# Kernel tuning notes

Measured on AMD Instinct MI355X. Metric: run time of the kernel, lower is better.

Reference implementation:

```python
import jax, jax.numpy as jnp
import numpy as np

N = 50000   # nodes
E = 800000  # edges
G = 64      # graphs in batch
H1, D1 = 2, 64   # gat1: 2 heads x 64
D2 = 32          # gat2: 1 head x 32
IN = 1
EPS = 1e-5


def _gat(h, src, dst, W, al, ar, Wres, bias, Hh, D):
    # DGL GATConv (eval mode): project, per-edge attention, edge softmax over dst, scatter-sum, residual + bias
    feat = (h @ W).reshape(N, Hh, D)                     # [N,H,D]
    el = jnp.sum(feat * al, axis=-1)                     # [N,H]
    er = jnp.sum(feat * ar, axis=-1)                     # [N,H]
    e = jax.nn.leaky_relu(el[src] + er[dst], 0.2)        # [E,H]
    m = jax.ops.segment_max(e, dst, num_segments=N)      # [N,H] (stable softmax)
    a = jnp.exp(e - m[dst])
    s = jax.ops.segment_sum(a, dst, num_segments=N)
    alpha = a / s[dst]                                   # [E,H]
    msg = feat[src] * alpha[:, :, None]                  # [E,H,D]
    rst = jax.ops.segment_sum(msg, dst, num_segments=N)  # [N,H,D]
    res = (h @ Wres).reshape(N, Hh, D)
    return rst + res + bias.reshape(1, Hh, D)


def _bn(x, gamma, beta, mean, var):
    return (x - mean) * jax.lax.rsqrt(var + EPS) * gamma + beta


def setup_inputs() -> dict:
    key = jax.random.key(0)
    ks = jax.random.split(key, 32)
    rn = lambda i, shape: jax.random.normal(ks[i], shape, jnp.float32) * 0.1
    inp = {
        'feat': jax.random.normal(ks[0], (N, IN), jnp.float32),
        'W1': rn(1, (IN, H1 * D1)), 'al1': rn(2, (H1, D1)), 'ar1': rn(3, (H1, D1)),
        'res1': rn(4, (IN, H1 * D1)), 'b1': rn(5, (H1 * D1,)),
        'g1_gamma': jnp.ones((H1 * D1,), jnp.float32), 'g1_beta': jnp.zeros((H1 * D1,), jnp.float32),
        'g1_mean': rn(6, (H1 * D1,)), 'g1_var': jax.random.uniform(ks[7], (H1 * D1,), jnp.float32) + 0.5,
        'W2': rn(8, (H1 * D1, D2)), 'al2': rn(9, (1, D2)), 'ar2': rn(10, (1, D2)),
        'res2': rn(11, (H1 * D1, D2)), 'b2': rn(12, (D2,)),
        'g2_gamma': jnp.ones((D2,), jnp.float32), 'g2_beta': jnp.zeros((D2,), jnp.float32),
        'g2_mean': rn(13, (D2,)), 'g2_var': jax.random.uniform(ks[14], (D2,), jnp.float32) + 0.5,
        'Wd1': rn(15, (D2, H1 * D1)), 'bd1': rn(16, (H1 * D1,)),
        'gd_gamma': jnp.ones((H1 * D1,), jnp.float32), 'gd_beta': jnp.zeros((H1 * D1,), jnp.float32),
        'gd_mean': rn(17, (H1 * D1,)), 'gd_var': jax.random.uniform(ks[18], (H1 * D1,), jnp.float32) + 0.5,
        'Wd2': rn(19, (H1 * D1, IN)), 'bd2': rn(20, (IN,)),
        'src': jax.random.randint(ks[21], (E,), 0, N, jnp.int32),
        'dst': jax.random.randint(ks[22], (E,), 0, N, jnp.int32),
        'graph_ids': jnp.sort(jax.random.randint(ks[23], (N,), 0, G, jnp.int32)),
    }
    return inp


def reference(feat, W1, al1, ar1, res1, b1, g1_gamma, g1_beta, g1_mean, g1_var,
              W2, al2, ar2, res2, b2, g2_gamma, g2_beta, g2_mean, g2_var,
              Wd1, bd1, gd_gamma, gd_beta, gd_mean, gd_var, Wd2, bd2,
              src, dst, graph_ids):
    h = _gat(feat, src, dst, W1, al1, ar1, res1, b1, H1, D1)   # [N,2,64]
    h = h.reshape(N, H1 * D1)
    h = jax.nn.relu(_bn(h, g1_gamma, g1_beta, g1_mean, g1_var))
    h = _gat(h, src, dst, W2, al2, ar2, res2, b2, 1, D2)       # [N,1,32]
    h = h.reshape(N, D2)
    h = jax.nn.relu(_bn(h, g2_gamma, g2_beta, g2_mean, g2_var))
    # dgl.mean_nodes over batched graphs
    counts = jax.ops.segment_sum(jnp.ones((N,), h.dtype), graph_ids, num_segments=G)
    graph_rep = jax.ops.segment_sum(h, graph_ids, num_segments=G) / jnp.maximum(counts, 1.0)[:, None]
    # decoder: Linear -> BN -> ReLU -> Linear (dropout off in eval)
    d = jax.nn.relu(_bn(h @ Wd1 + bd1, gd_gamma, gd_beta, gd_mean, gd_var))
    reconstruction = d @ Wd2 + bd2
    return graph_rep, reconstruction
```

## Files before the change

### kernel.cpp

```cpp
#include <hip/hip_runtime.h>
#include <hip/hip_bf16.h>
#include <hip/hip_fp16.h>

#define NN 50000
#define NE 800000
#define NG 64
#define C1 128
#define D2 32
#define CAP 32
#define NRANGE 4
#define RNG 12500
#define NCH 391
#define BN_EPS 1e-5f

#define CST_A   0
#define CST_B   2
#define CST_P   4
#define CST_Q   132
#define CST_R   260
#define CST_SC2 388
#define CST_RC2 420
#define CST_SD  452
#define CST_RD  580
#define CST_N   1024

#define UO_DEGP  0
#define UO_OVFC  800000
#define ZERO_UNITS 800016
#define UO_FLAG  800016
#define UO_CST   800032
#define UO_ESRC2 801056
#define UO_OVF   1601056
#define UO_FCAN  3201056
#define UO_F2    3251056
#define UO_RS2   4051056
#define UO_EL2   5651056
#define UO_ER2   5701056

typedef _Float16 h2vec __attribute__((ext_vector_type(2)));

__device__ __forceinline__ float lrelu(float x) { return fmaxf(x, 0.2f * x); }
__device__ __forceinline__ float bu2f(unsigned int u) {
    union { unsigned int i; float f; } v; v.i = (u & 0xFFFFu) << 16; return v.f;
}
__device__ __forceinline__ unsigned short f2bu(float f) {
    union { float f; unsigned int i; } v; v.f = f;
    unsigned int r = v.i + 0x7FFFu + ((v.i >> 16) & 1u);
    return (unsigned short)(r >> 16);
}
__device__ __forceinline__ unsigned int packh2(float a, float b) {
    h2vec h; h.x = (_Float16)a; h.y = (_Float16)b;
    union { h2vec h; unsigned int u; } v; v.h = h; return v.u;
}
__device__ __forceinline__ h2vec as_h2(unsigned int u) {
    union { unsigned int u; h2vec h; } v; v.u = u; return v.h;
}
__device__ __forceinline__ float ldw(const void* p, int i, int bf) {
    return bf ? bu2f(((const unsigned short*)p)[i]) : ((const float*)p)[i];
}
__device__ __forceinline__ int sniff64(const unsigned int* fw, int l) {
    int cnt = 0;
    for (int j = l; j < 256; j += 64) {
        unsigned int b = (fw[j] >> 8) & 0x7Fu;
        cnt += (b >= 0x3Au && b <= 0x41u) ? 1 : 0;
    }
#pragma unroll
    for (int m = 32; m >= 1; m >>= 1) cnt += __shfl_xor(cnt, m);
    return (cnt > 128) ? 1 : 0;
}

__global__ __launch_bounds__(256) void k_prep(
                       const void* __restrict__ feat, const int* __restrict__ dst,
                       const int* __restrict__ src,
                       float* __restrict__ fcan, int* __restrict__ degp,
                       unsigned short* __restrict__ esrc2,
                       int2* __restrict__ ovf, int* __restrict__ ovfc,
                       const void* W1, const void* al1, const void* ar1,
                       const void* res1, const void* b1,
                       const void* g1g, const void* g1b, const void* g1m, const void* g1v,
                       const void* b2v, const void* g2g, const void* g2b,
                       const void* g2m, const void* g2v,
                       const void* bd1, const void* gdg, const void* gdb,
                       const void* gdm, const void* gdv,
                       int* __restrict__ flag, float* __restrict__ cst) {
    __shared__ int sBf;
    int t = threadIdx.x;
    if (t < 64) {
        int b = sniff64((const unsigned int*)feat, t);
        if (t == 0) sBf = b;
    }
    __syncthreads();
    int bf = sBf;
    int r = blockIdx.x / NCH;
    int c = blockIdx.x % NCH;

    if (blockIdx.x == 0) {
        if (t == 0) *flag = bf;
        if (t < 128) {
            float w1v = ldw(W1, t, bf);
            float pa = w1v * ldw(al1, t, bf);
            float pb = w1v * ldw(ar1, t, bf);
#pragma unroll
            for (int m = 32; m >= 1; m >>= 1) { pa += __shfl_xor(pa, m); pb += __shfl_xor(pb, m); }
            if ((t & 63) == 0) { cst[CST_A + (t >> 6)] = pa; cst[CST_B + (t >> 6)] = pb; }
            float sc = rsqrtf(ldw(g1v, t, bf) + BN_EPS) * ldw(g1g, t, bf);
            cst[CST_P + t] = w1v * sc;
            cst[CST_Q + t] = ldw(res1, t, bf) * sc;
            cst[CST_R + t] = (ldw(b1, t, bf) - ldw(g1m, t, bf)) * sc + ldw(g1b, t, bf);
            if (t < D2) {
                float s2 = rsqrtf(ldw(g2v, t, bf) + BN_EPS) * ldw(g2g, t, bf);
                cst[CST_SC2 + t] = s2;
                cst[CST_RC2 + t] = (ldw(b2v, t, bf) - ldw(g2m, t, bf)) * s2 + ldw(g2b, t, bf);
            }
            float sd = rsqrtf(ldw(gdv, t, bf) + BN_EPS) * ldw(gdg, t, bf);
            cst[CST_SD + t] = sd;
            cst[CST_RD + t] = (ldw(bd1, t, bf) - ldw(gdm, t, bf)) * sd + ldw(gdb, t, bf);
        }
    }

    int lo = r * RNG, hi = lo + RNG;
#pragma unroll
    for (int j = 0; j < 8; ++j) {
        int k = c * 2048 + j * 256 + t;
        if (k < NE) {
            int d = dst[k];
            if (d >= lo && d < hi) {
                int slot = atomicAdd(&degp[d << 4], 1);
                if (slot < CAP) {
                    esrc2[d * CAP + slot] = (unsigned short)src[k];
                } else {
                    int p = atomicAdd(ovfc, 1);
                    ovf[p] = make_int2(d, src[k]);
                }
            }
        }
        if (r == 0 && k < NN) fcan[k] = ldw(feat, k, bf);
    }
}

__global__ __launch_bounds__(256) void k_layer1(
        const float* __restrict__ fcan, const void* W2, const void* res2,
        const void* al2, const void* ar2,
        const int* __restrict__ flag, const float* __restrict__ cst,
        const int* __restrict__ degp, const unsigned short* __restrict__ esrc2,
        const int2* __restrict__ ovf, const int* __restrict__ ovfc,
        unsigned short* __restrict__ F2, float* __restrict__ RS2,
        float* __restrict__ EL2, float* __restrict__ ER2) {
    __shared__ unsigned int sW2pk[32 * 66];
    __shared__ unsigned int sR2pk[32 * 66];
    __shared__ unsigned int sH1pk[32 * 66];
    __shared__ float sP[C1], sQ[C1], sR[C1];
    __shared__ float sAl[D2], sAr[D2];
    int t = threadIdx.x;
    int bf = *flag;
    for (int u = t; u < 2048; u += 256) {
        int cw = u >> 5, l2 = u & 31;
        sW2pk[l2 * 66 + cw] = packh2(ldw(W2, cw * D2 + l2, bf),
                                     ldw(W2, (cw + 64) * D2 + l2, bf));
        sR2pk[l2 * 66 + cw] = packh2(ldw(res2, cw * D2 + l2, bf),
                                     ldw(res2, (cw + 64) * D2 + l2, bf));
    }
    if (t < C1) { sP[t] = cst[CST_P + t]; sQ[t] = cst[CST_Q + t]; sR[t] = cst[CST_R + t]; }
    if (t < D2) { sAl[t] = ldw(al2, t, bf); sAr[t] = ldw(ar2, t, bf); }
    __syncthreads();

    int l = t & 31;
    int g = t >> 5;
    int base = blockIdx.x * 32;
    float A0 = cst[CST_A + 0], A1 = cst[CST_A + 1];
    float B0 = cst[CST_B + 0], B1 = cst[CST_B + 1];

    int dcap[4], draw[4];
    float fiK[4];
#pragma unroll
    for (int k = 0; k < 4; ++k) {
        int i = base + g * 4 + k;
        if (i < NN) {
            draw[k] = degp[i << 4];
            dcap[k] = draw[k] < CAP ? draw[k] : CAP;
            fiK[k] = fcan[i];
        } else { draw[k] = 0; dcap[k] = 0; fiK[k] = 0.0f; }
    }
    float S0[4], S1[4], N0[4], N1[4];
#pragma unroll
    for (int k = 0; k < 4; ++k) { S0[k] = S1[k] = N0[k] = N1[k] = 0.0f; }
    int sA[4];
#pragma unroll
    for (int k = 0; k < 4; ++k)
        sA[k] = (l < dcap[k]) ? (int)esrc2[(base + g * 4 + k) * CAP + l] : 0;
    float fA[4];
#pragma unroll
    for (int k = 0; k < 4; ++k) fA[k] = fcan[sA[k]];
#pragma unroll
    for (int k = 0; k < 4; ++k) {
        if (l < dcap[k]) {
            float w0 = __expf(lrelu(A0 * fA[k] + B0 * fiK[k]));
            float w1 = __expf(lrelu(A1 * fA[k] + B1 * fiK[k]));
            S0[k] += w0; N0[k] += w0 * fA[k];
            S1[k] += w1; N1[k] += w1 * fA[k];
        }
    }
#pragma unroll
    for (int k = 0; k < 4; ++k) {
        if (draw[k] > CAP) {
            int i = base + g * 4 + k;
            int novf = *ovfc;
            for (int p = l; p < novf; p += 32) {
                int2 o = ovf[p];
                if (o.x == i) {
                    float fs = fcan[o.y];
                    float w0 = __expf(lrelu(A0 * fs + B0 * fiK[k]));
                    float w1 = __expf(lrelu(A1 * fs + B1 * fiK[k]));
                    S0[k] += w0; N0[k] += w0 * fs;
                    S1[k] += w1; N1[k] += w1 * fs;
                }
            }
        }
    }
#pragma unroll
    for (int m = 16; m >= 1; m >>= 1) {
#pragma unroll
        for (int k = 0; k < 4; ++k) {
            S0[k] += __shfl_xor(S0[k], m); N0[k] += __shfl_xor(N0[k], m);
            S1[k] += __shfl_xor(S1[k], m); N1[k] += __shfl_xor(N1[k], m);
        }
    }
#pragma unroll
    for (int k = 0; k < 4; ++k) {
        int slot = g * 4 + k;
        float T0 = S0[k] > 0.0f ? N0[k] / S0[k] : 0.0f;
        float T1 = S1[k] > 0.0f ? N1[k] / S1[k] : 0.0f;
        float h0  = fmaxf(sP[l]      * T0 + sQ[l]      * fiK[k] + sR[l],      0.0f);
        float h1v = fmaxf(sP[l + 32] * T0 + sQ[l + 32] * fiK[k] + sR[l + 32], 0.0f);
        float h2v = fmaxf(sP[l + 64] * T1 + sQ[l + 64] * fiK[k] + sR[l + 64], 0.0f);
        float h3v = fmaxf(sP[l + 96] * T1 + sQ[l + 96] * fiK[k] + sR[l + 96], 0.0f);
        sH1pk[slot * 66 + l]      = packh2(h0,  h2v);
        sH1pk[slot * 66 + l + 32] = packh2(h1v, h3v);
    }
    __syncthreads();

    int w = t >> 6;
    int half = (t >> 5) & 1;
    int nb0 = w * 8 + half * 4;
    float aF[4] = {0.f, 0.f, 0.f, 0.f}, aR[4] = {0.f, 0.f, 0.f, 0.f};
    for (int cw = 0; cw < 64; cw += 2) {
        uint2 wq = *(const uint2*)&sW2pk[l * 66 + cw];
        uint2 rq = *(const uint2*)&sR2pk[l * 66 + cw];
#pragma unroll
        for (int n = 0; n < 4; ++n) {
            uint2 hq = *(const uint2*)&sH1pk[(nb0 + n) * 66 + cw];
            aF[n] = __builtin_amdgcn_fdot2(as_h2(hq.x), as_h2(wq.x),
                    __builtin_amdgcn_fdot2(as_h2(hq.y), as_h2(wq.y), aF[n], false), false);
            aR[n] = __builtin_amdgcn_fdot2(as_h2(hq.x), as_h2(rq.x),
                    __builtin_amdgcn_fdot2(as_h2(hq.y), as_h2(rq.y), aR[n], false), false);
        }
    }
#pragma unroll
    for (int n = 0; n < 4; ++n) {
        int i = base + nb0 + n;
        if (i < NN) {
            float elp = aF[n] * sAl[l], erp = aF[n] * sAr[l];
#pragma unroll
            for (int m = 16; m >= 1; m >>= 1) {
                elp += __shfl_xor(elp, m);
                erp += __shfl_xor(erp, m);
            }
            if (l == 0) { EL2[i] = elp; ER2[i] = erp; }
            F2[(size_t)i * D2 + l]  = f2bu(aF[n]);
            RS2[(size_t)i * D2 + l] = aR[n];
        }
    }
}

__global__ __launch_bounds__(256, 8) void k_final(
        const void* Wd1, const void* Wd2, const void* bd2,
        const int* __restrict__ flag, const float* __restrict__ cst,
        const int* __restrict__ degp, const unsigned short* __restrict__ esrc2,
        const int2* __restrict__ ovf, const int* __restrict__ ovfc,
        const unsigned short* __restrict__ F2, float* __restrict__ RS2,
        const float* __restrict__ EL2, const float* __restrict__ ER2,
        float* __restrict__ out) {
    __shared__ float sWd1x[4096];
    __shared__ unsigned int sWS[8 * 64];
    int t = threadIdx.x;
    int bf = *flag;
    for (int u = t; u < 4096; u += 256) {
        int d = u >> 7, lq = (u >> 2) & 31, j = u & 3;
        sWd1x[u] = ldw(Wd1, d * C1 + j * 32 + lq, bf);
    }

    int i = (blockIdx.x * 256 + t) >> 5;
    int l = t & 31;
    int nb = t >> 5;

    float sc2 = cst[CST_SC2 + l], rc2 = cst[CST_RC2 + l];
    float sd0 = cst[CST_SD + l],      rd0 = cst[CST_RD + l];
    float sd1 = cst[CST_SD + l + 32], rd1 = cst[CST_RD + l + 32];
    float sd2 = cst[CST_SD + l + 64], rd2 = cst[CST_RD + l + 64];
    float sd3 = cst[CST_SD + l + 96], rd3 = cst[CST_RD + l + 96];
    float wd2_0 = ldw(Wd2, l, bf),      wd2_1 = ldw(Wd2, l + 32, bf);
    float wd2_2 = ldw(Wd2, l + 64, bf), wd2_3 = ldw(Wd2, l + 96, bf);
    __syncthreads();

    float eri = ER2[i];
    int dr = degp[i << 4];
    int dcap = dr < CAP ? dr : CAP;
    const unsigned short* row = &esrc2[i * CAP];

    int sMy = 0; float wMy = 0.0f;
    if (l < dcap) {
        sMy = (int)row[l];
        wMy = __expf(lrelu(EL2[sMy] + eri));
    }
    float S = wMy;
#pragma unroll
    for (int m = 16; m >= 1; m >>= 1) S += __shfl_xor(S, m);
    sWS[nb * 64 + 2 * l]     = __float_as_uint(wMy);
    sWS[nb * 64 + 2 * l + 1] = (unsigned int)sMy;

    float aF0 = 0.f, aF1 = 0.f, aF2 = 0.f, aF3 = 0.f;
    int e = 0;
    for (; e + 3 < dcap; e += 4) {
        uint2 p0 = *(const uint2*)&sWS[nb * 64 + 2 * e];
        uint2 p1 = *(const uint2*)&sWS[nb * 64 + 2 * (e + 1)];
        uint2 p2 = *(const uint2*)&sWS[nb * 64 + 2 * (e + 2)];
        uint2 p3 = *(const uint2*)&sWS[nb * 64 + 2 * (e + 3)];
        float v0 = bu2f(F2[(size_t)p0.y * D2 + l]);
        float v1 = bu2f(F2[(size_t)p1.y * D2 + l]);
        float v2 = bu2f(F2[(size_t)p2.y * D2 + l]);
        float v3 = bu2f(F2[(size_t)p3.y * D2 + l]);
        aF0 = fmaf(__uint_as_float(p0.x), v0, aF0);
        aF1 = fmaf(__uint_as_float(p1.x), v1, aF1);
        aF2 = fmaf(__uint_as_float(p2.x), v2, aF2);
        aF3 = fmaf(__uint_as_float(p3.x), v3, aF3);
    }
    for (; e < dcap; ++e) {
        uint2 p = *(const uint2*)&sWS[nb * 64 + 2 * e];
        aF0 = fmaf(__uint_as_float(p.x), bu2f(F2[(size_t)p.y * D2 + l]), aF0);
    }
    if (dr > CAP) {
        int novf = *ovfc;
        for (int p = 0; p < novf; ++p) {
            int2 o = ovf[p];
            if (o.x == i) {
                float wA = __expf(lrelu(EL2[o.y] + eri));
                S += wA;
                aF0 = fmaf(wA, bu2f(F2[(size_t)o.y * D2 + l]), aF0);
            }
        }
    }
    float aF = (aF0 + aF1) + (aF2 + aF3);
    float inv = S > 0.0f ? 1.0f / S : 0.0f;

    float h2 = fmaxf((aF * inv + RS2[(size_t)i * D2 + l]) * sc2 + rc2, 0.0f);
    RS2[(size_t)i * D2 + l] = h2;

    const float4* Wx = (const float4*)sWd1x;
    float ac0 = 0.0f, ac1 = 0.0f, ac2 = 0.0f, ac3 = 0.0f;
#pragma unroll
    for (int d = 0; d < D2; ++d) {
        float h = __shfl(h2, d, 32);
        float4 wv = Wx[d * 32 + l];
        ac0 = fmaf(h, wv.x, ac0);
        ac1 = fmaf(h, wv.y, ac1);
        ac2 = fmaf(h, wv.z, ac2);
        ac3 = fmaf(h, wv.w, ac3);
    }
    float rec = fmaxf(ac0 * sd0 + rd0, 0.0f) * wd2_0
              + fmaxf(ac1 * sd1 + rd1, 0.0f) * wd2_1
              + fmaxf(ac2 * sd2 + rd2, 0.0f) * wd2_2
              + fmaxf(ac3 * sd3 + rd3, 0.0f) * wd2_3;
#pragma unroll
    for (int m = 16; m >= 1; m >>= 1) rec += __shfl_xor(rec, m);
    if (l == 0) out[NG * D2 + i] = rec + ldw(bd2, 0, bf);
}

__global__ __launch_bounds__(256) void k_pool2(const int* __restrict__ gid,
                                               const float* __restrict__ H2,
                                               float* __restrict__ out) {
    __shared__ int sLo, sHi;
    __shared__ float sAcc[32 * 32];
    int g = blockIdx.x;
    int t = threadIdx.x;
    if (t == 0) {
        int lo = 0, hi = NN;
        while (lo < hi) { int m = (lo + hi) >> 1; if (gid[m] < g) lo = m + 1; else hi = m; }
        sLo = lo;
        lo = 0; hi = NN;
        while (lo < hi) { int m = (lo + hi) >> 1; if (gid[m] < g + 1) lo = m + 1; else hi = m; }
        sHi = lo;
    }
    __syncthreads();
    int lo = sLo, hi = sHi;
    int q = t & 7;
    int row = t >> 3;
    float4 acc = make_float4(0.f, 0.f, 0.f, 0.f);
    for (int i = lo + row; i < hi; i += 32) {
        float4 v = ((const float4*)&H2[(size_t)i * D2])[q];
        acc.x += v.x; acc.y += v.y; acc.z += v.z; acc.w += v.w;
    }
    *(float4*)&sAcc[row * 32 + 4 * q] = acc;
    __syncthreads();
    if (t < 32) {
        float a = 0.0f;
        for (int r = 0; r < 32; ++r) a += sAcc[r * 32 + t];
        float c = (float)(hi - lo);
        out[g * D2 + t] = a / fmaxf(c, 1.0f);
    }
}

extern "C" void kernel_launch(void* const* d_in, const int* in_sizes, int n_in,
                              void* d_out, int out_size, void* d_ws, size_t ws_size,
                              hipStream_t stream) {
    const void* feat = d_in[0];
    const void* W1 = d_in[1];  const void* al1 = d_in[2];  const void* ar1 = d_in[3];
    const void* res1 = d_in[4]; const void* b1 = d_in[5];
    const void* g1g = d_in[6]; const void* g1b = d_in[7];
    const void* g1m = d_in[8]; const void* g1v = d_in[9];
    const void* W2 = d_in[10]; const void* al2 = d_in[11]; const void* ar2 = d_in[12];
    const void* res2 = d_in[13]; const void* b2v = d_in[14];
    const void* g2g = d_in[15]; const void* g2b = d_in[16];
    const void* g2m = d_in[17]; const void* g2v = d_in[18];
    const void* Wd1 = d_in[19]; const void* bd1 = d_in[20];
    const void* gdg = d_in[21]; const void* gdb = d_in[22];
    const void* gdm = d_in[23]; const void* gdv = d_in[24];
    const void* Wd2 = d_in[25]; const void* bd2 = d_in[26];
    const int* src = (const int*)d_in[27];
    const int* dst = (const int*)d_in[28];
    const int* gid = (const int*)d_in[29];

    unsigned int* wsu = (unsigned int*)d_ws;
    int* degp   = (int*)(wsu + UO_DEGP);
    int* ovfc   = (int*)(wsu + UO_OVFC);
    int* flag   = (int*)(wsu + UO_FLAG);
    float* cst  = (float*)(wsu + UO_CST);
    unsigned short* esrc2 = (unsigned short*)(wsu + UO_ESRC2);
    int2* ovf   = (int2*)(wsu + UO_OVF);
    float* fcan = (float*)(wsu + UO_FCAN);
    unsigned short* F2 = (unsigned short*)(wsu + UO_F2);
    float* RS2  = (float*)(wsu + UO_RS2);
    float* EL2  = (float*)(wsu + UO_EL2);
    float* ER2  = (float*)(wsu + UO_ER2);

    hipMemsetAsync(d_ws, 0, (size_t)ZERO_UNITS * 4, stream);

    k_prep<<<NCH * NRANGE, 256, 0, stream>>>(feat, dst, src, fcan, degp,
                                             esrc2, ovf, ovfc,
                                             W1, al1, ar1, res1, b1,
                                             g1g, g1b, g1m, g1v,
                                             b2v, g2g, g2b, g2m, g2v,
                                             bd1, gdg, gdb, gdm, gdv,
                                             flag, cst);

    k_layer1<<<(NN + 31) / 32, 256, 0, stream>>>(fcan, W2, res2, al2, ar2, flag, cst,
                                                 degp, esrc2, ovf, ovfc,
                                                 F2, RS2, EL2, ER2);

    k_final<<<(NN * 32) / 256, 256, 0, stream>>>(Wd1, Wd2, bd2, flag, cst,
                                                 degp, esrc2, ovf, ovfc,
                                                 F2, RS2, EL2, ER2,
                                                 (float*)d_out);

    k_pool2<<<NG, 256, 0, stream>>>(gid, RS2, (float*)d_out);
}
```

Measured before the change: 250.8 us.

## Single-pass edge bucketing and persistent grid-stride layer-1 blocks

```diff
diff --git a/kernel.cpp b/kernel.cpp
--- a/kernel.cpp
+++ b/kernel.cpp
@@ -8,9 +8,9 @@
 #define C1 128
 #define D2 32
 #define CAP 32
-#define NRANGE 4
-#define RNG 12500
-#define NCH 391
+#define EPT 4
+#define PBLK 782
+#define L1BLK 512
 #define BN_EPS 1e-5f
 
 #define CST_A   0
@@ -91,8 +91,6 @@
     }
     __syncthreads();
     int bf = sBf;
-    int r = blockIdx.x / NCH;
-    int c = blockIdx.x % NCH;
 
     if (blockIdx.x == 0) {
         if (t == 0) *flag = bf;
@@ -118,23 +116,34 @@
         }
     }
 
-    int lo = r * RNG, hi = lo + RNG;
-#pragma unroll
-    for (int j = 0; j < 8; ++j) {
-        int k = c * 2048 + j * 256 + t;
-        if (k < NE) {
-            int d = dst[k];
-            if (d >= lo && d < hi) {
-                int slot = atomicAdd(&degp[d << 4], 1);
-                if (slot < CAP) {
-                    esrc2[d * CAP + slot] = (unsigned short)src[k];
-                } else {
-                    int p = atomicAdd(ovfc, 1);
-                    ovf[p] = make_int2(d, src[k]);
-                }
-            }
-        }
-        if (r == 0 && k < NN) fcan[k] = ldw(feat, k, bf);
+    for (int k = blockIdx.x * 256 + t; k < NN; k += PBLK * 256)
+        fcan[k] = ldw(feat, k, bf);
+
+    int base = blockIdx.x * (256 * EPT) + t;
+    int dv[EPT], sv[EPT];
+    bool vv[EPT];
+#pragma unroll
+    for (int j = 0; j < EPT; ++j) {
+        int k = base + j * 256;
+        vv[j] = (k < NE);
+        dv[j] = vv[j] ? dst[k] : 0;
+        sv[j] = vv[j] ? src[k] : 0;
+    }
+    int slot[EPT];
+#pragma unroll
+    for (int j = 0; j < EPT; ++j)
+        if (vv[j]) slot[j] = atomicAdd(&degp[dv[j] << 4], 1);
+    __builtin_amdgcn_sched_barrier(0);
+#pragma unroll
+    for (int j = 0; j < EPT; ++j) {
+        if (vv[j]) {
+            if (slot[j] < CAP) {
+                esrc2[dv[j] * CAP + slot[j]] = (unsigned short)sv[j];
+            } else {
+                int p = atomicAdd(ovfc, 1);
+                ovf[p] = make_int2(dv[j], sv[j]);
+            }
+        }
     }
 }
 
@@ -162,113 +171,113 @@
     }
     if (t < C1) { sP[t] = cst[CST_P + t]; sQ[t] = cst[CST_Q + t]; sR[t] = cst[CST_R + t]; }
     if (t < D2) { sAl[t] = ldw(al2, t, bf); sAr[t] = ldw(ar2, t, bf); }
+    float A0 = cst[CST_A + 0], A1 = cst[CST_A + 1];
+    float B0 = cst[CST_B + 0], B1 = cst[CST_B + 1];
     __syncthreads();
 
     int l = t & 31;
     int g = t >> 5;
-    int base = blockIdx.x * 32;
-    float A0 = cst[CST_A + 0], A1 = cst[CST_A + 1];
-    float B0 = cst[CST_B + 0], B1 = cst[CST_B + 1];
-
-    int dcap[4], draw[4];
-    float fiK[4];
-#pragma unroll
-    for (int k = 0; k < 4; ++k) {
-        int i = base + g * 4 + k;
-        if (i < NN) {
-            draw[k] = degp[i << 4];
-            dcap[k] = draw[k] < CAP ? draw[k] : CAP;
-            fiK[k] = fcan[i];
-        } else { draw[k] = 0; dcap[k] = 0; fiK[k] = 0.0f; }
-    }
-    float S0[4], S1[4], N0[4], N1[4];
-#pragma unroll
-    for (int k = 0; k < 4; ++k) { S0[k] = S1[k] = N0[k] = N1[k] = 0.0f; }
-    int sA[4];
-#pragma unroll
-    for (int k = 0; k < 4; ++k)
-        sA[k] = (l < dcap[k]) ? (int)esrc2[(base + g * 4 + k) * CAP + l] : 0;
-    float fA[4];
-#pragma unroll
-    for (int k = 0; k < 4; ++k) fA[k] = fcan[sA[k]];
-#pragma unroll
-    for (int k = 0; k < 4; ++k) {
-        if (l < dcap[k]) {
-            float w0 = __expf(lrelu(A0 * fA[k] + B0 * fiK[k]));
-            float w1 = __expf(lrelu(A1 * fA[k] + B1 * fiK[k]));
-            S0[k] += w0; N0[k] += w0 * fA[k];
-            S1[k] += w1; N1[k] += w1 * fA[k];
-        }
-    }
-#pragma unroll
-    for (int k = 0; k < 4; ++k) {
-        if (draw[k] > CAP) {
+    int w = t >> 6, half = (t >> 5) & 1, nb0 = w * 8 + half * 4;
+
+    for (int base = blockIdx.x * 32; base < NN; base += L1BLK * 32) {
+        int dcap[4], draw[4];
+        float fiK[4];
+#pragma unroll
+        for (int k = 0; k < 4; ++k) {
             int i = base + g * 4 + k;
-            int novf = *ovfc;
-            for (int p = l; p < novf; p += 32) {
-                int2 o = ovf[p];
-                if (o.x == i) {
-                    float fs = fcan[o.y];
-                    float w0 = __expf(lrelu(A0 * fs + B0 * fiK[k]));
-                    float w1 = __expf(lrelu(A1 * fs + B1 * fiK[k]));
-                    S0[k] += w0; N0[k] += w0 * fs;
-                    S1[k] += w1; N1[k] += w1 * fs;
+            if (i < NN) {
+                draw[k] = degp[i << 4];
+                dcap[k] = draw[k] < CAP ? draw[k] : CAP;
+                fiK[k] = fcan[i];
+            } else { draw[k] = 0; dcap[k] = 0; fiK[k] = 0.0f; }
+        }
+        float S0[4], S1[4], N0[4], N1[4];
+#pragma unroll
+        for (int k = 0; k < 4; ++k) { S0[k] = S1[k] = N0[k] = N1[k] = 0.0f; }
+        int sA[4];
+#pragma unroll
+        for (int k = 0; k < 4; ++k)
+            sA[k] = (l < dcap[k]) ? (int)esrc2[(base + g * 4 + k) * CAP + l] : 0;
+        float fA[4];
+#pragma unroll
+        for (int k = 0; k < 4; ++k) fA[k] = fcan[sA[k]];
+#pragma unroll
+        for (int k = 0; k < 4; ++k) {
+            if (l < dcap[k]) {
+                float w0 = __expf(lrelu(A0 * fA[k] + B0 * fiK[k]));
+                float w1 = __expf(lrelu(A1 * fA[k] + B1 * fiK[k]));
+                S0[k] += w0; N0[k] += w0 * fA[k];
+                S1[k] += w1; N1[k] += w1 * fA[k];
+            }
+        }
+#pragma unroll
+        for (int k = 0; k < 4; ++k) {
+            if (draw[k] > CAP) {
+                int i = base + g * 4 + k;
+                int novf = *ovfc;
+                for (int p = l; p < novf; p += 32) {
+                    int2 o = ovf[p];
+                    if (o.x == i) {
+                        float fs = fcan[o.y];
+                        float w0 = __expf(lrelu(A0 * fs + B0 * fiK[k]));
+                        float w1 = __expf(lrelu(A1 * fs + B1 * fiK[k]));
+                        S0[k] += w0; N0[k] += w0 * fs;
+                        S1[k] += w1; N1[k] += w1 * fs;
+                    }
                 }
             }
         }
-    }
-#pragma unroll
-    for (int m = 16; m >= 1; m >>= 1) {
+#pragma unroll
+        for (int m = 16; m >= 1; m >>= 1) {
+#pragma unroll
+            for (int k = 0; k < 4; ++k) {
+                S0[k] += __shfl_xor(S0[k], m); N0[k] += __shfl_xor(N0[k], m);
+                S1[k] += __shfl_xor(S1[k], m); N1[k] += __shfl_xor(N1[k], m);
+            }
+        }
 #pragma unroll
         for (int k = 0; k < 4; ++k) {
-            S0[k] += __shfl_xor(S0[k], m); N0[k] += __shfl_xor(N0[k], m);
-            S1[k] += __shfl_xor(S1[k], m); N1[k] += __shfl_xor(N1[k], m);
-        }
-    }
-#pragma unroll
-    for (int k = 0; k < 4; ++k) {
-        int slot = g * 4 + k;
-        float T0 = S0[k] > 0.0f ? N0[k] / S0[k] : 0.0f;
-        float T1 = S1[k] > 0.0f ? N1[k] / S1[k] : 0.0f;
-        float h0  = fmaxf(sP[l]      * T0 + sQ[l]      * fiK[k] + sR[l],      0.0f);
-        float h1v = fmaxf(sP[l + 32] * T0 + sQ[l + 32] * fiK[k] + sR[l + 32], 0.0f);
-        float h2v = fmaxf(sP[l + 64] * T1 + sQ[l + 64] * fiK[k] + sR[l + 64], 0.0f);
-        float h3v = fmaxf(sP[l + 96] * T1 + sQ[l + 96] * fiK[k] + sR[l + 96], 0.0f);
-        sH1pk[slot * 66 + l]      = packh2(h0,  h2v);
-        sH1pk[slot * 66 + l + 32] = packh2(h1v, h3v);
-    }
-    __syncthreads();
-
-    int w = t >> 6;
-    int half = (t >> 5) & 1;
-    int nb0 = w * 8 + half * 4;
-    float aF[4] = {0.f, 0.f, 0.f, 0.f}, aR[4] = {0.f, 0.f, 0.f, 0.f};
-    for (int cw = 0; cw < 64; cw += 2) {
-        uint2 wq = *(const uint2*)&sW2pk[l * 66 + cw];
-        uint2 rq = *(const uint2*)&sR2pk[l * 66 + cw];
+            int slot = g * 4 + k;
+            float T0 = S0[k] > 0.0f ? N0[k] / S0[k] : 0.0f;
+            float T1 = S1[k] > 0.0f ? N1[k] / S1[k] : 0.0f;
+            float h0  = fmaxf(sP[l]      * T0 + sQ[l]      * fiK[k] + sR[l],      0.0f);
+            float h1v = fmaxf(sP[l + 32] * T0 + sQ[l + 32] * fiK[k] + sR[l + 32], 0.0f);
+            float h2v = fmaxf(sP[l + 64] * T1 + sQ[l + 64] * fiK[k] + sR[l + 64], 0.0f);
+            float h3v = fmaxf(sP[l + 96] * T1 + sQ[l + 96] * fiK[k] + sR[l + 96], 0.0f);
+            sH1pk[slot * 66 + l]      = packh2(h0,  h2v);
+            sH1pk[slot * 66 + l + 32] = packh2(h1v, h3v);
+        }
+        __syncthreads();
+
+        float aF[4] = {0.f, 0.f, 0.f, 0.f}, aR[4] = {0.f, 0.f, 0.f, 0.f};
+        for (int cw = 0; cw < 64; cw += 2) {
+            uint2 wq = *(const uint2*)&sW2pk[l * 66 + cw];
+            uint2 rq = *(const uint2*)&sR2pk[l * 66 + cw];
+#pragma unroll
+            for (int n = 0; n < 4; ++n) {
+                uint2 hq = *(const uint2*)&sH1pk[(nb0 + n) * 66 + cw];
+                aF[n] = __builtin_amdgcn_fdot2(as_h2(hq.x), as_h2(wq.x),
+                        __builtin_amdgcn_fdot2(as_h2(hq.y), as_h2(wq.y), aF[n], false), false);
+                aR[n] = __builtin_amdgcn_fdot2(as_h2(hq.x), as_h2(rq.x),
+                        __builtin_amdgcn_fdot2(as_h2(hq.y), as_h2(rq.y), aR[n], false), false);
+            }
+        }
 #pragma unroll
         for (int n = 0; n < 4; ++n) {
-            uint2 hq = *(const uint2*)&sH1pk[(nb0 + n) * 66 + cw];
-            aF[n] = __builtin_amdgcn_fdot2(as_h2(hq.x), as_h2(wq.x),
-                    __builtin_amdgcn_fdot2(as_h2(hq.y), as_h2(wq.y), aF[n], false), false);
-            aR[n] = __builtin_amdgcn_fdot2(as_h2(hq.x), as_h2(rq.x),
-                    __builtin_amdgcn_fdot2(as_h2(hq.y), as_h2(rq.y), aR[n], false), false);
-        }
-    }
-#pragma unroll
-    for (int n = 0; n < 4; ++n) {
-        int i = base + nb0 + n;
-        if (i < NN) {
-            float elp = aF[n] * sAl[l], erp = aF[n] * sAr[l];
-#pragma unroll
-            for (int m = 16; m >= 1; m >>= 1) {
-                elp += __shfl_xor(elp, m);
-                erp += __shfl_xor(erp, m);
-            }
-            if (l == 0) { EL2[i] = elp; ER2[i] = erp; }
-            F2[(size_t)i * D2 + l]  = f2bu(aF[n]);
-            RS2[(size_t)i * D2 + l] = aR[n];
-        }
+            int i = base + nb0 + n;
+            if (i < NN) {
+                float elp = aF[n] * sAl[l], erp = aF[n] * sAr[l];
+#pragma unroll
+                for (int m = 16; m >= 1; m >>= 1) {
+                    elp += __shfl_xor(elp, m);
+                    erp += __shfl_xor(erp, m);
+                }
+                if (l == 0) { EL2[i] = elp; ER2[i] = erp; }
+                F2[(size_t)i * D2 + l]  = f2bu(aF[n]);
+                RS2[(size_t)i * D2 + l] = aR[n];
+            }
+        }
+        __syncthreads();
     }
 }
 
@@ -444,17 +453,17 @@
 
     hipMemsetAsync(d_ws, 0, (size_t)ZERO_UNITS * 4, stream);
 
-    k_prep<<<NCH * NRANGE, 256, 0, stream>>>(feat, dst, src, fcan, degp,
-                                             esrc2, ovf, ovfc,
-                                             W1, al1, ar1, res1, b1,
-                                             g1g, g1b, g1m, g1v,
-                                             b2v, g2g, g2b, g2m, g2v,
-                                             bd1, gdg, gdb, gdm, gdv,
-                                             flag, cst);
-
-    k_layer1<<<(NN + 31) / 32, 256, 0, stream>>>(fcan, W2, res2, al2, ar2, flag, cst,
-                                                 degp, esrc2, ovf, ovfc,
-                                                 F2, RS2, EL2, ER2);
+    k_prep<<<PBLK, 256, 0, stream>>>(feat, dst, src, fcan, degp,
+                                     esrc2, ovf, ovfc,
+                                     W1, al1, ar1, res1, b1,
+                                     g1g, g1b, g1m, g1v,
+                                     b2v, g2g, g2b, g2m, g2v,
+                                     bd1, gdg, gdb, gdm, gdv,
+                                     flag, cst);
+
+    k_layer1<<<L1BLK, 256, 0, stream>>>(fcan, W2, res2, al2, ar2, flag, cst,
+                                        degp, esrc2, ovf, ovfc,
+                                        F2, RS2, EL2, ER2);
 
     k_final<<<(NN * 32) / 256, 256, 0, stream>>>(Wd1, Wd2, bd2, flag, cst,
                                                  degp, esrc2, ovf, ovfc,
```

New measurement: 251.5 us. Within noise of the previous version (+0.3%).
